# Optimization experiments

Measured on AMD Instinct MI355X. Metric: run time of the kernel, lower is better.

The kernel has to match this reference:

```python
import jax, jax.numpy as jnp
import numpy as np

B, N, R, C = 8, 300, 36, 256
IOU_THR, CONF_THR = 0.7, 0.3
OUT, SR = 7, 2  # roi_align output 7x7, sampling_ratio fixed to 2 (torchvision adaptive -1 approximated)


def pairwise_iou(a, b):
    area_a = (a[:, 2] - a[:, 0]) * (a[:, 3] - a[:, 1])
    area_b = (b[:, 2] - b[:, 0]) * (b[:, 3] - b[:, 1])
    lt = jnp.maximum(a[:, None, :2], b[None, :, :2])
    rb = jnp.minimum(a[:, None, 2:], b[None, :, 2:])
    wh = jnp.clip(rb - lt, 0.0)
    inter = wh[..., 0] * wh[..., 1]
    return inter / (area_a[:, None] + area_b[None, :] - inter + 1e-9)


def nms_select(boxes, scores):
    # confidence filter -> hard NMS -> keep top R in score order (fixed-shape, masked)
    s = jnp.where(scores > CONF_THR, scores, -jnp.inf)
    order = jnp.argsort(-s)
    b = boxes[order]
    v = s[order] > -jnp.inf
    iou = pairwise_iou(b, b)
    idx = jnp.arange(N)
    def body(i, keep):
        sup = keep[i] & (iou[i] > IOU_THR) & (idx > i)
        return keep & (~sup)
    keep = jax.lax.fori_loop(0, N, body, v)
    sel = jnp.argsort((~keep).astype(jnp.int32))[:R]  # stable sort: kept boxes first, score-ordered
    return b[sel], keep[sel]


def pooled_roi(feat, boxes):
    # roi_align(7x7, sampling_ratio=2, spatial_scale=1, aligned=False) followed by
    # AdaptiveAvgPool2d((1,1)) == mean of the 14x14 bilinear samples per ROI (fused here).
    _, H, W = feat.shape
    x1, y1, x2, y2 = boxes[:, 0], boxes[:, 1], boxes[:, 2], boxes[:, 3]
    rw = jnp.maximum(x2 - x1, 1.0)
    rh = jnp.maximum(y2 - y1, 1.0)
    g = (jnp.arange(OUT * SR) + 0.5) / (OUT * SR)  # sample centers in [0,1)
    Y = (y1[:, None] + rh[:, None] * g)[:, :, None]  # [R,G,1]
    X = (x1[:, None] + rw[:, None] * g)[:, None, :]  # [R,1,G]
    oob = (Y < -1.0) | (Y > H) | (X < -1.0) | (X > W)
    y = jnp.clip(Y, 0.0, H - 1)
    x = jnp.clip(X, 0.0, W - 1)
    y0 = jnp.floor(y).astype(jnp.int32)
    x0 = jnp.floor(x).astype(jnp.int32)
    y1i = jnp.minimum(y0 + 1, H - 1)
    x1i = jnp.minimum(x0 + 1, W - 1)
    ly = y - y0
    lx = x - x0
    v = (feat[:, y0, x0] * (1 - ly) * (1 - lx) + feat[:, y0, x1i] * (1 - ly) * lx
         + feat[:, y1i, x0] * ly * (1 - lx) + feat[:, y1i, x1i] * ly * lx)  # [C,R,G,G]
    v = jnp.where(oob[None], 0.0, v)
    return v.mean(axis=(2, 3)).T  # [R,C]


def setup_inputs() -> dict:
    key = jax.random.key(0)
    kc, kw, ks, k0, k1, k2, k3 = jax.random.split(key, 7)
    cxy = jax.random.uniform(kc, (B, N, 2), minval=0.0, maxval=200.0)
    wh = jax.random.uniform(kw, (B, N, 2), minval=8.0, maxval=120.0)
    boxes = jnp.concatenate([jnp.maximum(cxy - wh / 2, 0.0), cxy + wh / 2], axis=-1)
    scores = jax.random.uniform(ks, (B, N))
    feat0 = jax.random.normal(k0, (B, C, 200, 200), dtype=jnp.float32)
    feat1 = jax.random.normal(k1, (B, C, 100, 100), dtype=jnp.float32)
    feat2 = jax.random.normal(k2, (B, C, 50, 50), dtype=jnp.float32)
    feat3 = jax.random.normal(k3, (B, C, 25, 25), dtype=jnp.float32)
    return {"boxes": boxes, "scores": scores, "feat0": feat0, "feat1": feat1,
            "feat2": feat2, "feat3": feat3}


def reference(boxes, scores, feat0, feat1, feat2, feat3):
    sel_boxes, sel_valid = jax.vmap(nms_select)(boxes, scores)  # [B,R,4], [B,R]
    d = sel_boxes[..., 2:] - sel_boxes[..., :2]
    sizes = jnp.sqrt(jnp.maximum((d ** 2).sum(-1), 1e-12))
    lv = jnp.clip(jnp.floor(4.0 + jnp.log2(sizes / 224.0 * 4.0)), 2.0, 5.0).astype(jnp.int32) - 2
    out = jnp.zeros((B, R, C), boxes.dtype)
    for l, feat in enumerate([feat0, feat1, feat2, feat3]):
        pooled = jax.vmap(pooled_roi)(feat, sel_boxes)  # [B,R,C]
        mask = (lv == l) & sel_valid
        out = jnp.where(mask[..., None], pooled, out)
    return out  # [B, top_rois, 256]; rows for invalid ROIs are zero
```

## Files before the change

kernel.cpp:

```cpp
#include <hip/hip_runtime.h>
#include <math.h>

#define BB   8
#define NB   300
#define RSEL 36
#define NCH  256
#define NW   10
#define IOU_THR  0.7f
#define CONF_THR 0.3f
#define WSTR 128


__global__ __launch_bounds__(256) void nms_kernel(
    const float* __restrict__ boxes, const float* __restrict__ scores,
    float* __restrict__ ws)
{
    const int b   = blockIdx.x;
    const int tid = threadIdx.x;

    __shared__ float ss[NB];
    __shared__ float sbx[NB][4];
    __shared__ unsigned int supp[NB][NW];
    __shared__ unsigned int keepw[NW];
    __shared__ int kept_total;

    const float NEG_INF = -__builtin_inff();

    for (int i = tid; i < NB; i += blockDim.x) {
        float sc = scores[b * NB + i];
        ss[i] = (sc > CONF_THR) ? sc : NEG_INF;
    }
    for (int t = tid; t < NB * NW; t += blockDim.x)
        ((unsigned int*)supp)[t] = 0u;
    if (tid < NW) keepw[tid] = 0u;
    __syncthreads();

    for (int i = tid; i < NB; i += blockDim.x) {
        float si = ss[i];
        int r = 0;
        for (int j = 0; j < NB; ++j) {
            float sj = ss[j];
            r += (sj > si) || (sj == si && j < i);
        }
        sbx[r][0] = boxes[(b * NB + i) * 4 + 0];
        sbx[r][1] = boxes[(b * NB + i) * 4 + 1];
        sbx[r][2] = boxes[(b * NB + i) * 4 + 2];
        sbx[r][3] = boxes[(b * NB + i) * 4 + 3];
        if (si > NEG_INF) atomicOr(&keepw[r >> 5], 1u << (r & 31));
    }
    __syncthreads();

    for (int t = tid; t < NB * NB; t += blockDim.x) {
        int i = t / NB, j = t % NB;
        if (j <= i) continue;
        float ax1 = sbx[i][0], ay1 = sbx[i][1], ax2 = sbx[i][2], ay2 = sbx[i][3];
        float bx1 = sbx[j][0], by1 = sbx[j][1], bx2 = sbx[j][2], by2 = sbx[j][3];
        float area_a = (ax2 - ax1) * (ay2 - ay1);
        float area_b = (bx2 - bx1) * (by2 - by1);
        float ltx = fmaxf(ax1, bx1), lty = fmaxf(ay1, by1);
        float rbx = fminf(ax2, bx2), rby = fminf(ay2, by2);
        float wx = fmaxf(rbx - ltx, 0.0f), wy = fmaxf(rby - lty, 0.0f);
        float inter = wx * wy;
        float iou = inter / (area_a + area_b - inter + 1e-9f);
        if (iou > IOU_THR) atomicOr(&supp[i][j >> 5], 1u << (j & 31));
    }
    __syncthreads();

    if (tid == 0) {
        unsigned int kp[NW];
#pragma unroll
        for (int k = 0; k < NW; ++k) kp[k] = keepw[k];
        for (int i = 0; i < NB; ++i) {
            if ((kp[i >> 5] >> (i & 31)) & 1u) {
#pragma unroll
                for (int k = 0; k < NW; ++k) kp[k] &= ~supp[i][k];
            }
        }
        int tot = 0;
#pragma unroll
        for (int k = 0; k < NW; ++k) { keepw[k] = kp[k]; tot += __popc(kp[k]); }
        kept_total = tot;
    }
    __syncthreads();

    for (int i = tid; i < NB; i += blockDim.x) {
        int w = i >> 5, bt = i & 31;
        int kbit = (keepw[w] >> bt) & 1;
        int pre_kept = 0;
        for (int k = 0; k < w; ++k) pre_kept += __popc(keepw[k]);
        pre_kept += __popc(keepw[w] & ((1u << bt) - 1u));
        int pos = kbit ? pre_kept : (kept_total + (i - pre_kept));
        if (pos >= RSEL) continue;

        float* o = ws + (size_t)(b * RSEL + pos) * WSTR;
        for (int k = 0; k < WSTR; ++k) o[k] = 0.0f;
        if (!kbit) continue;

        float bx1 = sbx[i][0], by1 = sbx[i][1], bx2 = sbx[i][2], by2 = sbx[i][3];
        float dx = bx2 - bx1, dy = by2 - by1;
        float sz = sqrtf(fmaxf(dx * dx + dy * dy, 1e-12f));
        float l  = floorf(4.0f + log2f(sz * (4.0f / 224.0f)));
        l = fminf(fmaxf(l, 2.0f), 5.0f) - 2.0f;
        int lvl = (int)l;
        int H = (lvl == 0) ? 200 : ((lvl == 1) ? 100 : ((lvl == 2) ? 50 : 25));
        float Hf = (float)H;

        o[0] = 1.0f;
        o[1] = l;

        int ridx[28]; float rwt[28]; int nr = 0;
        float rh = fmaxf(dy, 1.0f);
        for (int s = 0; s < 14; ++s) {
            float g = (s + 0.5f) * (1.0f / 14.0f);
            float Y = by1 + rh * g;
            bool oob = (Y < -1.0f) || (Y > Hf);
            float yc = fminf(fmaxf(Y, 0.0f), Hf - 1.0f);
            int y0 = (int)floorf(yc);
            int y1i = min(y0 + 1, H - 1);
            float ly = yc - (float)y0;
            float w0 = oob ? 0.0f : (1.0f - ly);
            float w1 = oob ? 0.0f : ly;
            if (w0 != 0.0f) {
                int m = 0; for (; m < nr; ++m) if (ridx[m] == y0) break;
                if (m == nr) { ridx[nr] = y0; rwt[nr] = w0; ++nr; } else rwt[m] += w0;
            }
            if (w1 != 0.0f) {
                int m = 0; for (; m < nr; ++m) if (ridx[m] == y1i) break;
                if (m == nr) { ridx[nr] = y1i; rwt[nr] = w1; ++nr; } else rwt[m] += w1;
            }
        }
        o[2] = (float)nr;
        for (int m = 0; m < nr; ++m) {
            o[8 + m]  = (float)ridx[m];
            o[36 + m] = rwt[m] * (1.0f / 196.0f);
        }

        float rw = fmaxf(dx, 1.0f);
        int xmn = 1 << 30, xmx = -1;
        for (int s = 0; s < 14; ++s) {
            float g = (s + 0.5f) * (1.0f / 14.0f);
            float X = bx1 + rw * g;
            bool oob = (X < -1.0f) || (X > Hf);
            if (oob) continue;
            float xc = fminf(fmaxf(X, 0.0f), Hf - 1.0f);
            int x0 = (int)floorf(xc);
            int x1i = min(x0 + 1, H - 1);
            float lx = xc - (float)x0;
            if ((1.0f - lx) != 0.0f) { xmn = min(xmn, x0);  xmx = max(xmx, x0);  }
            if (lx != 0.0f)          { xmn = min(xmn, x1i); xmx = max(xmx, x1i); }
        }
        int ce = (xmx >= xmn) ? (xmx - xmn + 1) : 0;
        if (ce > 64) ce = 64;
        o[3] = (float)ce;
        o[4] = (float)xmn;

        if (ce > 0) {
            for (int s = 0; s < 14; ++s) {
                float g = (s + 0.5f) * (1.0f / 14.0f);
                float X = bx1 + rw * g;
                bool oob = (X < -1.0f) || (X > Hf);
                if (oob) continue;
                float xc = fminf(fmaxf(X, 0.0f), Hf - 1.0f);
                int x0 = (int)floorf(xc);
                int x1i = min(x0 + 1, H - 1);
                float lx = xc - (float)x0;
                float w0 = 1.0f - lx;
                if (w0 != 0.0f) { int p = x0 - xmn;  if (p >= 0 && p < 64) o[64 + p] += w0; }
                if (lx != 0.0f) { int p = x1i - xmn; if (p >= 0 && p < 64) o[64 + p] += lx; }
            }
        }
    }
}

__global__ __launch_bounds__(256) void pool_kernel(
    const float* __restrict__ f0, const float* __restrict__ f1,
    const float* __restrict__ f2, const float* __restrict__ f3,
    const float* __restrict__ ws, float* __restrict__ out)
{
    const int br   = blockIdx.x;
    const int cg   = blockIdx.y;
    const int b    = br / RSEL;
    const int tid  = threadIdx.x;
    const int lane = tid & 63;
    const int wv   = tid >> 6;

    __shared__ float smeta[WSTR];
    for (int t = tid; t < WSTR; t += 256) smeta[t] = ws[(size_t)br * WSTR + t];
    __syncthreads();

    const size_t obase = (size_t)br * NCH + (size_t)cg * 64;
    if (smeta[0] == 0.0f) {
        if (tid < 64) out[obase + tid] = 0.0f;
        return;
    }

    const int lvl = (int)smeta[1];
    const int nr  = (int)smeta[2];
    const int ce  = (int)smeta[3];
    const int xmn = (int)smeta[4];

    const float* feat; int H;
    if      (lvl == 0) { feat = f0; H = 200; }
    else if (lvl == 1) { feat = f1; H = 100; }
    else if (lvl == 2) { feat = f2; H = 50;  }
    else               { feat = f3; H = 25;  }
    const int W = H;
    const size_t cstr = (size_t)H * W;

    const bool  ld  = (lane < ce);
    const float wxl = ld ? smeta[64 + lane] : 0.0f;

    const int c0 = cg * 64 + wv * 16;
    const float* fb = feat + ((size_t)b * NCH + c0) * cstr + xmn + lane;

    float acc[16];
#pragma unroll
    for (int u = 0; u < 16; ++u) acc[u] = 0.0f;

    for (int r = 0; r < nr; ++r) {
        int   row = (int)smeta[8 + r];
        float rwt = smeta[36 + r];
        const float* p = fb + (size_t)row * W;
#pragma unroll
        for (int u = 0; u < 16; ++u) {
            float v = 0.0f;
            if (ld) v = p[u * cstr];
            acc[u] = fmaf(rwt, v, acc[u]);
        }
    }

#pragma unroll
    for (int u = 0; u < 16; ++u) {
        float a = acc[u] * wxl;
        for (int off = 32; off; off >>= 1) a += __shfl_xor(a, off, 64);
        if (lane == 0) out[obase + wv * 16 + u] = a;
    }
}

extern "C" void kernel_launch(void* const* d_in, const int* in_sizes, int n_in,
                              void* d_out, int out_size, void* d_ws, size_t ws_size,
                              hipStream_t stream) {
    const float* boxes  = (const float*)d_in[0];
    const float* scores = (const float*)d_in[1];
    const float* f0     = (const float*)d_in[2];
    const float* f1     = (const float*)d_in[3];
    const float* f2     = (const float*)d_in[4];
    const float* f3     = (const float*)d_in[5];
    float* ws  = (float*)d_ws;
    float* out = (float*)d_out;

    nms_kernel<<<BB, 256, 0, stream>>>(boxes, scores, ws);
    dim3 pgrid(BB * RSEL, 4);
    pool_kernel<<<pgrid, 256, 0, stream>>>(f0, f1, f2, f3, ws, out);
}
```

Before: 564.7 us.

## Parallelize NMS kernel: 1024 threads, wave-wide greedy pass, cooperative workspace zeroing

Raises the NMS block size from 256 to 1024 threads, so the ranking and pairwise-IoU loops take fewer iterations per thread. The single-thread greedy suppression pass becomes a one-wave pass: each lane owns one keep word, the current word is broadcast with a shuffle, and the kept count is summed with a shuffle reduction. Each selected-ROI slot used to be zeroed by one thread writing 128 floats; the whole block now zeroes the workspace up front, and threads for non-kept boxes skip that slot entirely. The gain is bounded by how much of the total time the 8-block NMS kernel takes next to pool_kernel; larger blocks add more barrier and launch cost.

```diff
diff --git a/kernel.cpp b/kernel.cpp
--- a/kernel.cpp
+++ b/kernel.cpp
@@ -11,7 +11,9 @@
 #define WSTR 128
 
 
-__global__ __launch_bounds__(256) void nms_kernel(
+#define NMS_T 1024
+
+__global__ __launch_bounds__(NMS_T) void nms_kernel(
     const float* __restrict__ boxes, const float* __restrict__ scores,
     float* __restrict__ ws)
 {
@@ -26,16 +28,21 @@
 
     const float NEG_INF = -__builtin_inff();
 
-    for (int i = tid; i < NB; i += blockDim.x) {
+    {
+        float* wb = ws + (size_t)b * RSEL * WSTR;
+        for (int t = tid; t < RSEL * WSTR; t += NMS_T) wb[t] = 0.0f;
+    }
+
+    for (int i = tid; i < NB; i += NMS_T) {
         float sc = scores[b * NB + i];
         ss[i] = (sc > CONF_THR) ? sc : NEG_INF;
     }
-    for (int t = tid; t < NB * NW; t += blockDim.x)
+    for (int t = tid; t < NB * NW; t += NMS_T)
         ((unsigned int*)supp)[t] = 0u;
     if (tid < NW) keepw[tid] = 0u;
     __syncthreads();
 
-    for (int i = tid; i < NB; i += blockDim.x) {
+    for (int i = tid; i < NB; i += NMS_T) {
         float si = ss[i];
         int r = 0;
         for (int j = 0; j < NB; ++j) {
@@ -50,8 +57,8 @@
     }
     __syncthreads();
 
-    for (int t = tid; t < NB * NB; t += blockDim.x) {
-        int i = t / NB, j = t % NB;
+    for (int t = tid; t < NB * NB; t += NMS_T) {
+        int i = t / NB, j = t - i * NB;
         if (j <= i) continue;
         float ax1 = sbx[i][0], ay1 = sbx[i][1], ax2 = sbx[i][2], ay2 = sbx[i][3];
         float bx1 = sbx[j][0], by1 = sbx[j][1], bx2 = sbx[j][2], by2 = sbx[j][3];
@@ -66,24 +73,24 @@
     }
     __syncthreads();
 
-    if (tid == 0) {
-        unsigned int kp[NW];
-#pragma unroll
-        for (int k = 0; k < NW; ++k) kp[k] = keepw[k];
+    if (tid < 64) {
+        const int lane = tid;
+        unsigned int kpw = (lane < NW) ? keepw[lane] : 0u;
         for (int i = 0; i < NB; ++i) {
-            if ((kp[i >> 5] >> (i & 31)) & 1u) {
-#pragma unroll
-                for (int k = 0; k < NW; ++k) kp[k] &= ~supp[i][k];
-            }
-        }
-        int tot = 0;
-#pragma unroll
-        for (int k = 0; k < NW; ++k) { keepw[k] = kp[k]; tot += __popc(kp[k]); }
-        kept_total = tot;
-    }
-    __syncthreads();
-
-    for (int i = tid; i < NB; i += blockDim.x) {
+            unsigned int wrd = __shfl(kpw, i >> 5, 64);
+            if ((wrd >> (i & 31)) & 1u) {
+                unsigned int s = (lane < NW) ? supp[i][lane] : 0u;
+                kpw &= ~s;
+            }
+        }
+        if (lane < NW) keepw[lane] = kpw;
+        int tot = (lane < NW) ? __popc(kpw) : 0;
+        for (int off = 32; off; off >>= 1) tot += __shfl_xor(tot, off, 64);
+        if (lane == 0) kept_total = tot;
+    }
+    __syncthreads();
+
+    for (int i = tid; i < NB; i += NMS_T) {
         int w = i >> 5, bt = i & 31;
         int kbit = (keepw[w] >> bt) & 1;
         int pre_kept = 0;
@@ -91,10 +98,9 @@
         pre_kept += __popc(keepw[w] & ((1u << bt) - 1u));
         int pos = kbit ? pre_kept : (kept_total + (i - pre_kept));
         if (pos >= RSEL) continue;
+        if (!kbit) continue;
 
         float* o = ws + (size_t)(b * RSEL + pos) * WSTR;
-        for (int k = 0; k < WSTR; ++k) o[k] = 0.0f;
-        if (!kbit) continue;
 
         float bx1 = sbx[i][0], by1 = sbx[i][1], bx2 = sbx[i][2], by2 = sbx[i][3];
         float dx = bx2 - bx1, dy = by2 - by1;
@@ -249,7 +255,7 @@
     float* ws  = (float*)d_ws;
     float* out = (float*)d_out;
 
-    nms_kernel<<<BB, 256, 0, stream>>>(boxes, scores, ws);
+    nms_kernel<<<BB, NMS_T, 0, stream>>>(boxes, scores, ws);
     dim3 pgrid(BB * RSEL, 4);
     pool_kernel<<<pgrid, 256, 0, stream>>>(f0, f1, f2, f3, ws, out);
 }
```

New measurement: 555.8 us. No clear change (-1.6%).
